# Optimization experiments

Measured on AMD Instinct MI355X. Metric: run time of the kernel, lower is better.

The kernel has to match this reference:

```python
import jax, jax.numpy as jnp
import numpy as np


def setup_inputs() -> dict:
    key = jax.random.key(0)
    ks = jax.random.split(key, 8)
    B, C, H, W = 4, 256, 64, 64
    Cqk = C // 8
    s = 0.05
    return {
        "x": jax.random.normal(ks[0], (B, C, H, W), jnp.float32),
        "Wq": jax.random.normal(ks[1], (Cqk, C), jnp.float32) * s,
        "bq": jax.random.normal(ks[2], (Cqk,), jnp.float32) * s,
        "Wk": jax.random.normal(ks[3], (Cqk, C), jnp.float32) * s,
        "bk": jax.random.normal(ks[4], (Cqk,), jnp.float32) * s,
        "Wv": jax.random.normal(ks[5], (C, C), jnp.float32) * s,
        "bv": jax.random.normal(ks[6], (C,), jnp.float32) * s,
        "gamma": jax.random.normal(ks[7], (1,), jnp.float32),
    }


def reference(x, Wq, bq, Wk, bk, Wv, bv, gamma):
    B, C, H, W = x.shape
    N = H * W
    xf = x.reshape(B, C, N)                      # [B,C,N]
    # 1x1 convs == channel matmuls
    q = jnp.einsum('oc,bcn->bon', Wq, xf) + bq[None, :, None]   # [B,C/8,N]
    k = jnp.einsum('oc,bcn->bon', Wk, xf) + bk[None, :, None]   # [B,C/8,N]
    v = jnp.einsum('oc,bcn->bon', Wv, xf) + bv[None, :, None]   # [B,C,N]
    # scores[b,i,j] = <q[:,i], k[:,j]>; softmax over j (last dim)
    scores = jnp.einsum('bci,bcj->bij', q, k)                   # [B,N,N]
    attn = jax.nn.softmax(scores, axis=-1)
    # out[b,c,i] = sum_j v[b,c,j] * attn[b,i,j]
    out = jnp.einsum('bcj,bij->bci', v, attn).reshape(B, C, H, W)
    return gamma[0] * out + x
```

## Files before the change

kernel.cpp:

```cpp
#include <hip/hip_runtime.h>


#define B_ 4
#define C_ 256
#define N_ 4096
#define CQK 32
#define LOG2E 1.44269504088896340736f

typedef __attribute__((ext_vector_type(8))) short short8;
typedef __attribute__((ext_vector_type(4))) short short4v;
typedef __attribute__((ext_vector_type(2))) unsigned int uint2v;
typedef __attribute__((ext_vector_type(16))) float f32x16;
typedef __attribute__((ext_vector_type(4))) float f32x4;

__device__ __forceinline__ unsigned short f2bf(float f) {
  unsigned int u = __builtin_bit_cast(unsigned int, f);
  u = (u + 0x7fffu + ((u >> 16) & 1u)) >> 16;
  return (unsigned short)u;
}
__device__ __forceinline__ float bf2f(unsigned short s) {
  unsigned int u = ((unsigned int)s) << 16;
  return __builtin_bit_cast(float, u);
}
__device__ __forceinline__ short f32tof16(float f) {
  const _Float16 hf = (_Float16)f;
  return __builtin_bit_cast(short, hf);
}
__device__ __forceinline__ unsigned int cvtpk(float lo, float hi) {
  unsigned int r;
  asm("v_cvt_pk_bf16_f32 %0, %1, %2" : "=v"(r) : "v"(lo), "v"(hi));
  return r;
}
__device__ __forceinline__ f32x16 mfma16(short8 a, short8 b, f32x16 c) {
  return __builtin_amdgcn_mfma_f32_32x32x16_bf16(a, b, c, 0, 0, 0);
}
__device__ __forceinline__ int swz64(int row, int col) {
  return row * 64 + ((((col >> 3) ^ row) & 7) << 3) + (col & 7);
}

#define WAITCNT(s) asm volatile("s_waitcnt " s ::: "memory")
#define BARRIER()                         \
  do {                                    \
    __builtin_amdgcn_s_barrier();         \
    asm volatile("" ::: "memory");        \
  } while (0)

__global__ __launch_bounds__(256) void k_prep(
    const float* __restrict__ x, unsigned short* __restrict__ xthi,
    unsigned short* __restrict__ xtlo,
    const float* __restrict__ Wq, const float* __restrict__ Wk,
    const float* __restrict__ Wv,
    unsigned short* __restrict__ wqh, unsigned short* __restrict__ wql,
    unsigned short* __restrict__ wkh, unsigned short* __restrict__ wkl,
    unsigned short* __restrict__ wvh, unsigned short* __restrict__ wvl) {
  __shared__ __align__(16) float tile[64 * 65];
  const int bi = blockIdx.x;
  const int t = threadIdx.x;
  if (bi < 1024) {
    const int it = bi & 63, ct = (bi >> 6) & 3, b = bi >> 8;
    const int i0 = it * 64, c0 = ct * 64;
    {
      const int i = t & 63, cb = t >> 6;
#pragma unroll
      for (int z = 0; z < 16; ++z) {
        const int c = z * 4 + cb;
        tile[i * 65 + c] = x[(b * C_ + c0 + c) * N_ + i0 + i];
      }
    }
    __syncthreads();
    {
      const int ii = t >> 2, p = t & 3;
      short8 h0, h1, l0, l1;
#pragma unroll
      for (int e = 0; e < 16; ++e) {
        const float f = tile[ii * 65 + p * 16 + e];
        const unsigned short hb = f2bf(f);
        const unsigned short lb = f2bf(f - bf2f(hb));
        if (e < 8) { h0[e] = (short)hb; l0[e] = (short)lb; }
        else       { h1[e - 8] = (short)hb; l1[e - 8] = (short)lb; }
      }
      const int base = (b * N_ + i0 + ii) * C_ + c0 + p * 16;
      *(short8*)(xthi + base) = h0;
      *(short8*)(xthi + base + 8) = h1;
      *(short8*)(xtlo + base) = l0;
      *(short8*)(xtlo + base + 8) = l1;
    }
  } else {
    const int e = (bi - 1024) * 256 + t;
    const float* src; unsigned short *hi, *lo; int idx;
    if (e < 8192)        { src = Wq; hi = wqh; lo = wql; idx = e; }
    else if (e < 16384)  { src = Wk; hi = wkh; lo = wkl; idx = e - 8192; }
    else                 { src = Wv; hi = wvh; lo = wvl; idx = e - 16384; }
    float f = src[idx];
    if (e < 8192) f *= LOG2E;
    const unsigned short h = f2bf(f);
    hi[idx] = h;
    lo[idx] = f2bf(f - bf2f(h));
  }
}

__global__ __launch_bounds__(256) void k_proj(
    const unsigned short* __restrict__ wqh, const unsigned short* __restrict__ wql,
    const unsigned short* __restrict__ wkh, const unsigned short* __restrict__ wkl,
    const unsigned short* __restrict__ wvh, const unsigned short* __restrict__ wvl,
    const unsigned short* __restrict__ xthi, const unsigned short* __restrict__ xtlo,
    const float* __restrict__ bq, const float* __restrict__ bk,
    const float* __restrict__ bv,
    unsigned short* __restrict__ qhg, unsigned short* __restrict__ qlg,
    unsigned short* __restrict__ khg, unsigned short* __restrict__ klg,
    unsigned short* __restrict__ vg) {
  __shared__ __align__(16) char sm[33792];
  unsigned short* awh = (unsigned short*)sm;
  unsigned short* awl = awh + 4096;
  unsigned short* bxh = awl + 4096;
  unsigned short* bxl = bxh + 4096;
  float* qt = (float*)sm;

  const int it = blockIdx.x, ot = blockIdx.y, b = blockIdx.z;
  const int i0 = it * 64, o0 = ot * 64;
  const int t = threadIdx.x, lane = t & 63, w = t >> 6, h = lane >> 5;
  const int mb = w >> 1, nb = w & 1;
  const int srow = t >> 2, sp = t & 3;

  const int og = o0 + srow;
  const unsigned short *wh, *wl;
  if (og < 32)      { wh = wqh + og * C_;        wl = wql + og * C_; }
  else if (og < 64) { wh = wkh + (og - 32) * C_; wl = wkl + (og - 32) * C_; }
  else              { wh = wvh + (og - 64) * C_; wl = wvl + (og - 64) * C_; }
  const unsigned short* xh = xthi + (b * N_ + i0 + srow) * C_;
  const unsigned short* xl = xtlo + (b * N_ + i0 + srow) * C_;

  f32x16 acc;
#pragma unroll
  for (int e = 0; e < 16; ++e) acc[e] = 0.f;
  const int m = 32 * mb + (lane & 31);
  const int n = 32 * nb + (lane & 31);

  for (int kt = 0; kt < 4; ++kt) {
    const int cb = kt * 64 + sp * 16;
    *(short8*)&awh[swz64(srow, sp * 16)]     = *(const short8*)(wh + cb);
    *(short8*)&awh[swz64(srow, sp * 16 + 8)] = *(const short8*)(wh + cb + 8);
    *(short8*)&awl[swz64(srow, sp * 16)]     = *(const short8*)(wl + cb);
    *(short8*)&awl[swz64(srow, sp * 16 + 8)] = *(const short8*)(wl + cb + 8);
    *(short8*)&bxh[swz64(srow, sp * 16)]     = *(const short8*)(xh + cb);
    *(short8*)&bxh[swz64(srow, sp * 16 + 8)] = *(const short8*)(xh + cb + 8);
    *(short8*)&bxl[swz64(srow, sp * 16)]     = *(const short8*)(xl + cb);
    *(short8*)&bxl[swz64(srow, sp * 16 + 8)] = *(const short8*)(xl + cb + 8);
    __syncthreads();
#pragma unroll
    for (int kk = 0; kk < 4; ++kk) {
      const int kb = kk * 16 + h * 8;
      const short8 ah  = *(const short8*)&awh[swz64(m, kb)];
      const short8 al2 = *(const short8*)&awl[swz64(m, kb)];
      const short8 bh  = *(const short8*)&bxh[swz64(n, kb)];
      const short8 bl2 = *(const short8*)&bxl[swz64(n, kb)];
      acc = mfma16(ah, bh, acc);
      acc = mfma16(ah, bl2, acc);
      acc = mfma16(al2, bh, acc);
    }
    __syncthreads();
  }

  if (ot > 0) {
#pragma unroll
    for (int e = 0; e < 16; ++e) {
      const int r = 32 * mb + (e & 3) + 8 * (e >> 2) + 4 * h;
      const int oc = o0 - 64 + r;
      vg[(b * C_ + oc) * N_ + i0 + n] = f2bf(acc[e] + bv[oc]);
    }
  } else {
#pragma unroll
    for (int e = 0; e < 16; ++e) {
      const int r = 32 * mb + (e & 3) + 8 * (e >> 2) + 4 * h;
      const float bias = (r < 32) ? bq[r] * LOG2E : bk[r - 32];
      qt[r * 65 + n] = acc[e] + bias;
    }
    __syncthreads();
    const int ii = t >> 2;
    short8 hv0, hv1, lv0, lv1;
#pragma unroll
    for (int e = 0; e < 16; ++e) {
      const float f = qt[(sp * 16 + e) * 65 + ii];
      const unsigned short hb = f2bf(f);
      const unsigned short lb = f2bf(f - bf2f(hb));
      if (e < 8) { hv0[e] = (short)hb; lv0[e] = (short)lb; }
      else       { hv1[e - 8] = (short)hb; lv1[e - 8] = (short)lb; }
    }
    if (sp < 2) {
      const int base = (b * N_ + i0 + ii) * CQK + sp * 16;
      *(short8*)(qhg + base) = hv0; *(short8*)(qhg + base + 8) = hv1;
      *(short8*)(qlg + base) = lv0; *(short8*)(qlg + base + 8) = lv1;
    } else {
      const int base = (b * N_ + i0 + ii) * CQK + sp * 16 - 32;
      *(short8*)(khg + base) = hv0; *(short8*)(khg + base + 8) = hv1;
      *(short8*)(klg + base) = lv0; *(short8*)(klg + base + 8) = lv1;
    }
  }
}

__global__ __launch_bounds__(384, 3) void k_flash(
    const unsigned short* __restrict__ qhg, const unsigned short* __restrict__ qlg,
    const unsigned short* __restrict__ khg, const unsigned short* __restrict__ klg,
    const unsigned short* __restrict__ vg,
    unsigned short* __restrict__ Opart, float* __restrict__ mlpart) {
  __shared__ __align__(16) char sm[16928];
  char* Pb0 = sm;
  char* Pb1 = sm + 8192;
  float* alphaA = (float*)(sm + 16384);
  float* chgF = (float*)(sm + 16896);

  const int blk = blockIdx.x;
  const int b = (blk >> 1) & 3;
  const int half = blk & 1;
  const int qt_ = blk >> 3;
  const int q0 = qt_ * 64;
  const int jbase = half * 2048;
  const int t = threadIdx.x, lane = t & 63, w = t >> 6, h = lane >> 5;
  const int l31 = lane & 31;

  if (w < 4) {
    const int c0 = 64 * w + l31;
    const unsigned short* vsrc0 = vg + (size_t)(b * C_ + c0) * N_ + jbase + h * 8;
    const unsigned short* vsrc1 = vsrc0 + (size_t)32 * N_;
    f32x16 acc0, acc1, acc2, acc3;
#pragma unroll
    for (int e = 0; e < 16; ++e) {
      acc0[e] = 0.f; acc1[e] = 0.f; acc2[e] = 0.f; acc3[e] = 0.f;
    }
    short8 vf0[4], vf1[4];
#pragma unroll
    for (int kk = 0; kk < 4; ++kk) {
      vf0[kk] = *(const short8*)(vsrc0 + kk * 16);
      vf1[kk] = *(const short8*)(vsrc1 + kk * 16);
    }
    WAITCNT("lgkmcnt(0)");
    BARRIER();

#pragma unroll 2
    for (int kt = 0; kt < 32; ++kt) {
      const char* pb = (kt & 1) ? Pb1 : Pb0;
      const float* alp = alphaA + (kt & 1) * 64;
      const float cA = chgF[(kt & 1) * 2];
      const float cB = chgF[(kt & 1) * 2 + 1];
      if (cA != 0.f) {
#pragma unroll
        for (int eq = 0; eq < 4; ++eq) {
          const f32x4 av = *(const f32x4*)(alp + 8 * eq + 4 * h);
#pragma unroll
          for (int q = 0; q < 4; ++q) {
            acc0[4 * eq + q] *= av[q];
            acc2[4 * eq + q] *= av[q];
          }
        }
      }
      if (cB != 0.f) {
#pragma unroll
        for (int eq = 0; eq < 4; ++eq) {
          const f32x4 av = *(const f32x4*)(alp + 32 + 8 * eq + 4 * h);
#pragma unroll
          for (int q = 0; q < 4; ++q) {
            acc1[4 * eq + q] *= av[q];
            acc3[4 * eq + q] *= av[q];
          }
        }
      }
      __builtin_amdgcn_s_setprio(1);
#pragma unroll
      for (int kk = 0; kk < 4; ++kk) {
        const int phys = (2 * kk + h) ^ (l31 & 7);
        const short8 pa0 = *(const short8*)(pb + l31 * 128 + phys * 16);
        const short8 pa1 = *(const short8*)(pb + (32 + l31) * 128 + phys * 16);
        acc0 = mfma16(pa0, vf0[kk], acc0);
        acc1 = mfma16(pa1, vf0[kk], acc1);
        acc2 = mfma16(pa0, vf1[kk], acc2);
        acc3 = mfma16(pa1, vf1[kk], acc3);
      }
      __builtin_amdgcn_s_setprio(0);
      if (kt + 1 < 32) {
#pragma unroll
        for (int kk = 0; kk < 4; ++kk) {
          vf0[kk] = *(const short8*)(vsrc0 + (kt + 1) * 64 + kk * 16);
          vf1[kk] = *(const short8*)(vsrc1 + (kt + 1) * 64 + kk * 16);
        }
      }
      WAITCNT("lgkmcnt(0)");
      BARRIER();
    }
    {
      unsigned short* dst = Opart + (size_t)blk * 16384 + (w * 64 + lane) * 64;
      short8 o[8];
#pragma unroll
      for (int e = 0; e < 8; ++e) {
        o[0][e] = f32tof16(acc0[e]);      o[1][e] = f32tof16(acc0[8 + e]);
        o[2][e] = f32tof16(acc1[e]);      o[3][e] = f32tof16(acc1[8 + e]);
        o[4][e] = f32tof16(acc2[e]);      o[5][e] = f32tof16(acc2[8 + e]);
        o[6][e] = f32tof16(acc3[e]);      o[7][e] = f32tof16(acc3[8 + e]);
      }
#pragma unroll
      for (int q = 0; q < 8; ++q) *(short8*)(dst + 8 * q) = o[q];
    }
  } else {
    const int sw = w - 4;
    const int srow = sw * 32 + l31;
    short8 qfh[2], qfl[2];
    {
      const unsigned short* qph = qhg + (size_t)(b * N_ + q0 + srow) * CQK + h * 8;
      const unsigned short* qpl = qlg + (size_t)(b * N_ + q0 + srow) * CQK + h * 8;
#pragma unroll
      for (int kk = 0; kk < 2; ++kk) {
        qfh[kk] = *(const short8*)(qph + kk * 16);
        qfl[kk] = *(const short8*)(qpl + kk * 16);
      }
    }
    const unsigned short* kph = khg + (size_t)(b * N_ + jbase + l31) * CQK + h * 8;
    const unsigned short* kpl = klg + (size_t)(b * N_ + jbase + l31) * CQK + h * 8;
    short8 kfh[2][2], kfl[2][2];
    float m_run = -1e30f, l_run = 0.f;

    auto loadK = [&](int tau) {
#pragma unroll
      for (int jt = 0; jt < 2; ++jt)
#pragma unroll
        for (int kk = 0; kk < 2; ++kk) {
          kfh[jt][kk] = *(const short8*)(kph + tau * 2048 + jt * 1024 + kk * 16);
          kfl[jt][kk] = *(const short8*)(kpl + tau * 2048 + jt * 1024 + kk * 16);
        }
    };
    auto s_step = [&](int tau) {
      f32x16 s0, s1;
#pragma unroll
      for (int e = 0; e < 16; ++e) { s0[e] = 0.f; s1[e] = 0.f; }
      __builtin_amdgcn_s_setprio(1);
#pragma unroll
      for (int kk = 0; kk < 2; ++kk) {
        s0 = mfma16(kfh[0][kk], qfh[kk], s0);
        s0 = mfma16(kfh[0][kk], qfl[kk], s0);
        s0 = mfma16(kfl[0][kk], qfh[kk], s0);
        s1 = mfma16(kfh[1][kk], qfh[kk], s1);
        s1 = mfma16(kfh[1][kk], qfl[kk], s1);
        s1 = mfma16(kfl[1][kk], qfh[kk], s1);
      }
      __builtin_amdgcn_s_setprio(0);
      if (tau + 1 < 32) loadK(tau + 1);
      float mx8[8];
#pragma unroll
      for (int i2 = 0; i2 < 4; ++i2) {
        mx8[i2] = fmaxf(fmaxf(s0[4 * i2], s0[4 * i2 + 1]),
                        fmaxf(s0[4 * i2 + 2], s0[4 * i2 + 3]));
        mx8[4 + i2] = fmaxf(fmaxf(s1[4 * i2], s1[4 * i2 + 1]),
                            fmaxf(s1[4 * i2 + 2], s1[4 * i2 + 3]));
      }
      float mx = fmaxf(fmaxf(fmaxf(mx8[0], mx8[1]), fmaxf(mx8[2], mx8[3])),
                       fmaxf(fmaxf(mx8[4], mx8[5]), fmaxf(mx8[6], mx8[7])));
      mx = fmaxf(mx, __shfl_xor(mx, 32));
      const float mnew = fmaxf(m_run, mx);
      const bool up = mnew > m_run;
      const float al = __builtin_exp2f(m_run - mnew);
#pragma unroll
      for (int e = 0; e < 16; ++e) s0[e] = __builtin_exp2f(s0[e] - mnew);
#pragma unroll
      for (int e = 0; e < 16; ++e) s1[e] = __builtin_exp2f(s1[e] - mnew);
      float t8[8];
#pragma unroll
      for (int i2 = 0; i2 < 4; ++i2) {
        t8[i2] = (s0[4 * i2] + s0[4 * i2 + 1]) + (s0[4 * i2 + 2] + s0[4 * i2 + 3]);
        t8[4 + i2] = (s1[4 * i2] + s1[4 * i2 + 1]) + (s1[4 * i2 + 2] + s1[4 * i2 + 3]);
      }
      float ts = ((t8[0] + t8[1]) + (t8[2] + t8[3])) +
                 ((t8[4] + t8[5]) + (t8[6] + t8[7]));
      ts += __shfl_xor(ts, 32);
      l_run = l_run * al + ts;
      char* Pw = (tau & 1) ? Pb1 : Pb0;
#pragma unroll
      for (int q = 0; q < 4; ++q) {
        uint2v u0, u1;
        u0[0] = cvtpk(s0[4 * q], s0[4 * q + 1]);
        u0[1] = cvtpk(s0[4 * q + 2], s0[4 * q + 3]);
        u1[0] = cvtpk(s1[4 * q], s1[4 * q + 1]);
        u1[1] = cvtpk(s1[4 * q + 2], s1[4 * q + 3]);
        const int ph0 = q ^ (srow & 7);
        const int ph1 = (4 + q) ^ (srow & 7);
        *(uint2v*)(Pw + srow * 128 + ph0 * 16 + 8 * h) = u0;
        *(uint2v*)(Pw + srow * 128 + ph1 * 16 + 8 * h) = u1;
      }
      const unsigned long long ba = __ballot(up);
      if (h == 0) alphaA[(tau & 1) * 64 + srow] = al;
      if (lane == 0) chgF[(tau & 1) * 2 + sw] = ba ? 1.f : 0.f;
      m_run = mnew;
    };

    loadK(0);
    s_step(0);
    WAITCNT("lgkmcnt(0)");
    BARRIER();
#pragma unroll 2
    for (int kt = 0; kt < 32; ++kt) {
      if (kt + 1 < 32) s_step(kt + 1);
      WAITCNT("lgkmcnt(0)");
      BARRIER();
    }
    if (h == 0) {
      mlpart[blk * 128 + srow] = m_run;
      mlpart[blk * 128 + 64 + srow] = l_run;
    }
  }
}

__global__ __launch_bounds__(256) void k_combine(
    const unsigned short* __restrict__ Opart, const float* __restrict__ mlpart,
    const float* __restrict__ x, const float* __restrict__ gamma,
    float* __restrict__ out) {
  const int cb = blockIdx.x;
  const int b = cb & 3, qt_ = cb >> 2;
  const int q0 = qt_ * 64;
  const int blk1 = (qt_ << 3) | (b << 1);
  const int blk2 = blk1 | 1;
  const int t = threadIdx.x;
  const int i = t & 63, cg = t >> 6;

  const float m1 = mlpart[blk1 * 128 + i], l1 = mlpart[blk1 * 128 + 64 + i];
  const float m2 = mlpart[blk2 * 128 + i], l2 = mlpart[blk2 * 128 + 64 + i];
  const float M = fmaxf(m1, m2);
  const float w1 = __builtin_exp2f(m1 - M), w2 = __builtin_exp2f(m2 - M);
  const float inv = 1.f / (w1 * l1 + w2 * l2);
  const float gm = gamma[0];
  const float s1 = gm * w1 * inv, s2 = gm * w2 * inv;

  const int hh = (i >> 2) & 1;
  const int e = (i & 3) + 4 * ((i >> 3) & 3);
  const int rs = i >> 5;
  const unsigned short* p1 = Opart + (size_t)blk1 * 16384;
  const unsigned short* p2 = Opart + (size_t)blk2 * 16384;
#pragma unroll 4
  for (int c = cg; c < C_; c += 4) {
    const int off = (c >> 6) * 4096 + ((c & 31) + 32 * hh) * 64 +
                    (rs + 2 * ((c >> 5) & 1)) * 16 + e;
    const float o1 = (float)__builtin_bit_cast(_Float16, p1[off]);
    const float o2 = (float)__builtin_bit_cast(_Float16, p2[off]);
    const int g = (b * C_ + c) * N_ + q0 + i;
    out[g] = s1 * o1 + s2 * o2 + x[g];
  }
}

extern "C" void kernel_launch(void* const* d_in, const int* in_sizes, int n_in,
                              void* d_out, int out_size, void* d_ws, size_t ws_size,
                              hipStream_t stream) {
  const float* x     = (const float*)d_in[0];
  const float* Wq    = (const float*)d_in[1];
  const float* bq    = (const float*)d_in[2];
  const float* Wk    = (const float*)d_in[3];
  const float* bk    = (const float*)d_in[4];
  const float* Wv    = (const float*)d_in[5];
  const float* bv    = (const float*)d_in[6];
  const float* gamma = (const float*)d_in[7];
  float* out = (float*)d_out;
  (void)in_sizes; (void)n_in; (void)out_size; (void)ws_size;

  char* ws = (char*)d_ws;
  size_t off = 0;
  auto carve = [&](size_t bytes) -> char* {
    char* p = ws + off;
    off += (bytes + 255) & ~(size_t)255;
    return p;
  };
  unsigned short* xthi = (unsigned short*)carve((size_t)B_ * N_ * C_ * 2);
  unsigned short* xtlo = (unsigned short*)carve((size_t)B_ * N_ * C_ * 2);
  unsigned short* wqh  = (unsigned short*)carve(32 * 256 * 2);
  unsigned short* wql  = (unsigned short*)carve(32 * 256 * 2);
  unsigned short* wkh  = (unsigned short*)carve(32 * 256 * 2);
  unsigned short* wkl  = (unsigned short*)carve(32 * 256 * 2);
  unsigned short* wvh  = (unsigned short*)carve(256 * 256 * 2);
  unsigned short* wvl  = (unsigned short*)carve(256 * 256 * 2);
  unsigned short* qhg  = (unsigned short*)carve((size_t)B_ * N_ * CQK * 2);
  unsigned short* qlg  = (unsigned short*)carve((size_t)B_ * N_ * CQK * 2);
  unsigned short* khg  = (unsigned short*)carve((size_t)B_ * N_ * CQK * 2);
  unsigned short* klg  = (unsigned short*)carve((size_t)B_ * N_ * CQK * 2);
  unsigned short* vg   = (unsigned short*)carve((size_t)B_ * C_ * N_ * 2);
  unsigned short* Opart = (unsigned short*)carve((size_t)512 * 16384 * 2);
  float* mlpart = (float*)carve((size_t)512 * 128 * 4);

  k_prep<<<1344, 256, 0, stream>>>(x, xthi, xtlo, Wq, Wk, Wv,
                                   wqh, wql, wkh, wkl, wvh, wvl);
  k_proj<<<dim3(64, 5, B_), 256, 0, stream>>>(wqh, wql, wkh, wkl, wvh, wvl,
                                              xthi, xtlo, bq, bk, bv,
                                              qhg, qlg, khg, klg, vg);
  k_flash<<<512, 384, 0, stream>>>(qhg, qlg, khg, klg, vg, Opart, mlpart);
  k_combine<<<256, 256, 0, stream>>>(Opart, mlpart, x, gamma, out);
}
```

Measured before the change: 187.9 us.

## Fuse score and PV stages per wave, passing P through registers instead of LDS

Replaces the producer/consumer warp specialization (2 score waves writing P to LDS, 4 PV waves reading it with block barriers) with self-contained waves. Each wave computes its own 32-row score tile, converts P to bf16 in registers via lane shuffles, and feeds it directly into the PV MFMAs for 128 channels. This removes the LDS P buffers and the per-step barriers. In exchange, scores are recomputed twice per query row (once per channel half) and V loads are no longer prefetched. The Opart/mlpart layouts and the combine kernel's indexing are reworked to match.

```diff
diff --git a/kernel.cpp b/kernel.cpp
--- a/kernel.cpp
+++ b/kernel.cpp
@@ -9,7 +9,7 @@
 
 typedef __attribute__((ext_vector_type(8))) short short8;
 typedef __attribute__((ext_vector_type(4))) short short4v;
-typedef __attribute__((ext_vector_type(2))) unsigned int uint2v;
+typedef __attribute__((ext_vector_type(4))) unsigned int uint4v;
 typedef __attribute__((ext_vector_type(16))) float f32x16;
 typedef __attribute__((ext_vector_type(4))) float f32x4;
 
@@ -37,13 +37,6 @@
 __device__ __forceinline__ int swz64(int row, int col) {
   return row * 64 + ((((col >> 3) ^ row) & 7) << 3) + (col & 7);
 }
-
-#define WAITCNT(s) asm volatile("s_waitcnt " s ::: "memory")
-#define BARRIER()                         \
-  do {                                    \
-    __builtin_amdgcn_s_barrier();         \
-    asm volatile("" ::: "memory");        \
-  } while (0)
 
 __global__ __launch_bounds__(256) void k_prep(
     const float* __restrict__ x, unsigned short* __restrict__ xthi,
@@ -198,211 +191,219 @@
   }
 }
 
-__global__ __launch_bounds__(384, 3) void k_flash(
+__global__ __launch_bounds__(256, 2) void k_flash(
     const unsigned short* __restrict__ qhg, const unsigned short* __restrict__ qlg,
     const unsigned short* __restrict__ khg, const unsigned short* __restrict__ klg,
     const unsigned short* __restrict__ vg,
     unsigned short* __restrict__ Opart, float* __restrict__ mlpart) {
-  __shared__ __align__(16) char sm[16928];
-  char* Pb0 = sm;
-  char* Pb1 = sm + 8192;
-  float* alphaA = (float*)(sm + 16384);
-  float* chgF = (float*)(sm + 16896);
+  __shared__ float alphaW[4][32];
 
   const int blk = blockIdx.x;
-  const int b = (blk >> 1) & 3;
-  const int half = blk & 1;
-  const int qt_ = blk >> 3;
-  const int q0 = qt_ * 64;
-  const int jbase = half * 2048;
+  const int xs = blk & 7;
+  const int b = xs >> 1, s = xs & 1;
+  const int gl = blk >> 3;
   const int t = threadIdx.x, lane = t & 63, w = t >> 6, h = lane >> 5;
   const int l31 = lane & 31;
-
-  if (w < 4) {
-    const int c0 = 64 * w + l31;
-    const unsigned short* vsrc0 = vg + (size_t)(b * C_ + c0) * N_ + jbase + h * 8;
-    const unsigned short* vsrc1 = vsrc0 + (size_t)32 * N_;
-    f32x16 acc0, acc1, acc2, acc3;
-#pragma unroll
-    for (int e = 0; e < 16; ++e) {
-      acc0[e] = 0.f; acc1[e] = 0.f; acc2[e] = 0.f; acc3[e] = 0.f;
-    }
-    short8 vf0[4], vf1[4];
-#pragma unroll
-    for (int kk = 0; kk < 4; ++kk) {
-      vf0[kk] = *(const short8*)(vsrc0 + kk * 16);
-      vf1[kk] = *(const short8*)(vsrc1 + kk * 16);
-    }
-    WAITCNT("lgkmcnt(0)");
-    BARRIER();
-
-#pragma unroll 2
-    for (int kt = 0; kt < 32; ++kt) {
-      const char* pb = (kt & 1) ? Pb1 : Pb0;
-      const float* alp = alphaA + (kt & 1) * 64;
-      const float cA = chgF[(kt & 1) * 2];
-      const float cB = chgF[(kt & 1) * 2 + 1];
-      if (cA != 0.f) {
-#pragma unroll
-        for (int eq = 0; eq < 4; ++eq) {
-          const f32x4 av = *(const f32x4*)(alp + 8 * eq + 4 * h);
-#pragma unroll
-          for (int q = 0; q < 4; ++q) {
-            acc0[4 * eq + q] *= av[q];
-            acc2[4 * eq + q] *= av[q];
-          }
+  const int widx = gl * 4 + w;
+  const int qw = widx >> 1, ch = widx & 1;
+  const int srow = qw * 32 + l31;
+  const int jbase = s * 2048;
+
+  short8 qfh[2], qfl[2];
+  {
+    const unsigned short* qph = qhg + (size_t)(b * N_ + srow) * CQK + h * 8;
+    const unsigned short* qpl = qlg + (size_t)(b * N_ + srow) * CQK + h * 8;
+#pragma unroll
+    for (int kk = 0; kk < 2; ++kk) {
+      qfh[kk] = *(const short8*)(qph + kk * 16);
+      qfl[kk] = *(const short8*)(qpl + kk * 16);
+    }
+  }
+  const unsigned short* kph = khg + (size_t)(b * N_ + jbase + l31) * CQK + h * 8;
+  const unsigned short* kpl = klg + (size_t)(b * N_ + jbase + l31) * CQK + h * 8;
+  short8 kfh[2][2], kfl[2][2];
+  auto loadK = [&](int tau) {
+#pragma unroll
+    for (int jt = 0; jt < 2; ++jt)
+#pragma unroll
+      for (int kk = 0; kk < 2; ++kk) {
+        kfh[jt][kk] = *(const short8*)(kph + tau * 2048 + jt * 1024 + kk * 16);
+        kfl[jt][kk] = *(const short8*)(kpl + tau * 2048 + jt * 1024 + kk * 16);
+      }
+  };
+  loadK(0);
+  const unsigned short* vsr0 =
+      vg + (size_t)(b * C_ + ch * 128 + l31) * N_ + jbase + h * 8;
+
+  f32x16 acc0, acc1, acc2, acc3;
+#pragma unroll
+  for (int e = 0; e < 16; ++e) {
+    acc0[e] = 0.f; acc1[e] = 0.f; acc2[e] = 0.f; acc3[e] = 0.f;
+  }
+  float m_run = -1e30f, l_run = 0.f;
+
+  for (int kt = 0; kt < 32; ++kt) {
+    short8 vf0[4], vf1[4], vf2[4], vf3[4];
+#pragma unroll
+    for (int sl = 0; sl < 4; ++sl) {
+      vf0[sl] = *(const short8*)(vsr0 + (size_t)0 * 32 * N_ + kt * 64 + sl * 16);
+      vf1[sl] = *(const short8*)(vsr0 + (size_t)1 * 32 * N_ + kt * 64 + sl * 16);
+      vf2[sl] = *(const short8*)(vsr0 + (size_t)2 * 32 * N_ + kt * 64 + sl * 16);
+      vf3[sl] = *(const short8*)(vsr0 + (size_t)3 * 32 * N_ + kt * 64 + sl * 16);
+    }
+    f32x16 s0, s1;
+#pragma unroll
+    for (int e = 0; e < 16; ++e) { s0[e] = 0.f; s1[e] = 0.f; }
+    __builtin_amdgcn_s_setprio(1);
+#pragma unroll
+    for (int kk = 0; kk < 2; ++kk) {
+      s0 = mfma16(kfh[0][kk], qfh[kk], s0);
+      s0 = mfma16(kfh[0][kk], qfl[kk], s0);
+      s0 = mfma16(kfl[0][kk], qfh[kk], s0);
+      s1 = mfma16(kfh[1][kk], qfh[kk], s1);
+      s1 = mfma16(kfh[1][kk], qfl[kk], s1);
+      s1 = mfma16(kfl[1][kk], qfh[kk], s1);
+    }
+    __builtin_amdgcn_s_setprio(0);
+    if (kt + 1 < 32) loadK(kt + 1);
+    float mx8[8];
+#pragma unroll
+    for (int i2 = 0; i2 < 4; ++i2) {
+      mx8[i2] = fmaxf(fmaxf(s0[4 * i2], s0[4 * i2 + 1]),
+                      fmaxf(s0[4 * i2 + 2], s0[4 * i2 + 3]));
+      mx8[4 + i2] = fmaxf(fmaxf(s1[4 * i2], s1[4 * i2 + 1]),
+                          fmaxf(s1[4 * i2 + 2], s1[4 * i2 + 3]));
+    }
+    float mx = fmaxf(fmaxf(fmaxf(mx8[0], mx8[1]), fmaxf(mx8[2], mx8[3])),
+                     fmaxf(fmaxf(mx8[4], mx8[5]), fmaxf(mx8[6], mx8[7])));
+    mx = fmaxf(mx, __shfl_xor(mx, 32));
+    const float mnew = fmaxf(m_run, mx);
+    const unsigned long long ba = __ballot(mnew > m_run);
+    const float al = __builtin_exp2f(m_run - mnew);
+#pragma unroll
+    for (int e = 0; e < 16; ++e) s0[e] = __builtin_exp2f(s0[e] - mnew);
+#pragma unroll
+    for (int e = 0; e < 16; ++e) s1[e] = __builtin_exp2f(s1[e] - mnew);
+    float t8[8];
+#pragma unroll
+    for (int i2 = 0; i2 < 4; ++i2) {
+      t8[i2] = (s0[4 * i2] + s0[4 * i2 + 1]) + (s0[4 * i2 + 2] + s0[4 * i2 + 3]);
+      t8[4 + i2] = (s1[4 * i2] + s1[4 * i2 + 1]) + (s1[4 * i2 + 2] + s1[4 * i2 + 3]);
+    }
+    float ts = ((t8[0] + t8[1]) + (t8[2] + t8[3])) +
+               ((t8[4] + t8[5]) + (t8[6] + t8[7]));
+    ts += __shfl_xor(ts, 32);
+    l_run = l_run * al + ts;
+    m_run = mnew;
+    short8 pa0, pa1, pa2, pa3;
+    {
+      unsigned int w01 = cvtpk(s0[0], s0[1]),  w23 = cvtpk(s0[2], s0[3]);
+      unsigned int w45 = cvtpk(s0[4], s0[5]),  w67 = cvtpk(s0[6], s0[7]);
+      unsigned int w89 = cvtpk(s0[8], s0[9]),  wab = cvtpk(s0[10], s0[11]);
+      unsigned int wcd = cvtpk(s0[12], s0[13]), wef = cvtpk(s0[14], s0[15]);
+      unsigned int t01 = (unsigned)__shfl_xor((int)w01, 32);
+      unsigned int t23 = (unsigned)__shfl_xor((int)w23, 32);
+      unsigned int t45 = (unsigned)__shfl_xor((int)w45, 32);
+      unsigned int t67 = (unsigned)__shfl_xor((int)w67, 32);
+      unsigned int t89 = (unsigned)__shfl_xor((int)w89, 32);
+      unsigned int tab = (unsigned)__shfl_xor((int)wab, 32);
+      unsigned int tcd = (unsigned)__shfl_xor((int)wcd, 32);
+      unsigned int tef = (unsigned)__shfl_xor((int)wef, 32);
+      uint4v uA, uB;
+      uA[0] = h ? t45 : w01;  uA[1] = h ? t67 : w23;
+      uA[2] = h ? w45 : t01;  uA[3] = h ? w67 : t23;
+      uB[0] = h ? tcd : w89;  uB[1] = h ? tef : wab;
+      uB[2] = h ? wcd : t89;  uB[3] = h ? wef : tab;
+      pa0 = __builtin_bit_cast(short8, uA);
+      pa1 = __builtin_bit_cast(short8, uB);
+    }
+    {
+      unsigned int w01 = cvtpk(s1[0], s1[1]),  w23 = cvtpk(s1[2], s1[3]);
+      unsigned int w45 = cvtpk(s1[4], s1[5]),  w67 = cvtpk(s1[6], s1[7]);
+      unsigned int w89 = cvtpk(s1[8], s1[9]),  wab = cvtpk(s1[10], s1[11]);
+      unsigned int wcd = cvtpk(s1[12], s1[13]), wef = cvtpk(s1[14], s1[15]);
+      unsigned int t01 = (unsigned)__shfl_xor((int)w01, 32);
+      unsigned int t23 = (unsigned)__shfl_xor((int)w23, 32);
+      unsigned int t45 = (unsigned)__shfl_xor((int)w45, 32);
+      unsigned int t67 = (unsigned)__shfl_xor((int)w67, 32);
+      unsigned int t89 = (unsigned)__shfl_xor((int)w89, 32);
+      unsigned int tab = (unsigned)__shfl_xor((int)wab, 32);
+      unsigned int tcd = (unsigned)__shfl_xor((int)wcd, 32);
+      unsigned int tef = (unsigned)__shfl_xor((int)wef, 32);
+      uint4v uA, uB;
+      uA[0] = h ? t45 : w01;  uA[1] = h ? t67 : w23;
+      uA[2] = h ? w45 : t01;  uA[3] = h ? w67 : t23;
+      uB[0] = h ? tcd : w89;  uB[1] = h ? tef : wab;
+      uB[2] = h ? wcd : t89;  uB[3] = h ? wef : tab;
+      pa2 = __builtin_bit_cast(short8, uA);
+      pa3 = __builtin_bit_cast(short8, uB);
+    }
+    if (ba) {
+      if (h == 0) alphaW[w][l31] = al;
+#pragma unroll
+      for (int eq = 0; eq < 4; ++eq) {
+        const f32x4 av = *(const f32x4*)&alphaW[w][8 * eq + 4 * h];
+#pragma unroll
+        for (int q = 0; q < 4; ++q) {
+          acc0[4 * eq + q] *= av[q];
+          acc1[4 * eq + q] *= av[q];
+          acc2[4 * eq + q] *= av[q];
+          acc3[4 * eq + q] *= av[q];
         }
       }
-      if (cB != 0.f) {
-#pragma unroll
-        for (int eq = 0; eq < 4; ++eq) {
-          const f32x4 av = *(const f32x4*)(alp + 32 + 8 * eq + 4 * h);
-#pragma unroll
-          for (int q = 0; q < 4; ++q) {
-            acc1[4 * eq + q] *= av[q];
-            acc3[4 * eq + q] *= av[q];
-          }
-        }
-      }
-      __builtin_amdgcn_s_setprio(1);
-#pragma unroll
-      for (int kk = 0; kk < 4; ++kk) {
-        const int phys = (2 * kk + h) ^ (l31 & 7);
-        const short8 pa0 = *(const short8*)(pb + l31 * 128 + phys * 16);
-        const short8 pa1 = *(const short8*)(pb + (32 + l31) * 128 + phys * 16);
-        acc0 = mfma16(pa0, vf0[kk], acc0);
-        acc1 = mfma16(pa1, vf0[kk], acc1);
-        acc2 = mfma16(pa0, vf1[kk], acc2);
-        acc3 = mfma16(pa1, vf1[kk], acc3);
-      }
-      __builtin_amdgcn_s_setprio(0);
-      if (kt + 1 < 32) {
-#pragma unroll
-        for (int kk = 0; kk < 4; ++kk) {
-          vf0[kk] = *(const short8*)(vsrc0 + (kt + 1) * 64 + kk * 16);
-          vf1[kk] = *(const short8*)(vsrc1 + (kt + 1) * 64 + kk * 16);
-        }
-      }
-      WAITCNT("lgkmcnt(0)");
-      BARRIER();
-    }
-    {
-      unsigned short* dst = Opart + (size_t)blk * 16384 + (w * 64 + lane) * 64;
-      short8 o[8];
-#pragma unroll
-      for (int e = 0; e < 8; ++e) {
-        o[0][e] = f32tof16(acc0[e]);      o[1][e] = f32tof16(acc0[8 + e]);
-        o[2][e] = f32tof16(acc1[e]);      o[3][e] = f32tof16(acc1[8 + e]);
-        o[4][e] = f32tof16(acc2[e]);      o[5][e] = f32tof16(acc2[8 + e]);
-        o[6][e] = f32tof16(acc3[e]);      o[7][e] = f32tof16(acc3[8 + e]);
-      }
-#pragma unroll
-      for (int q = 0; q < 8; ++q) *(short8*)(dst + 8 * q) = o[q];
-    }
-  } else {
-    const int sw = w - 4;
-    const int srow = sw * 32 + l31;
-    short8 qfh[2], qfl[2];
-    {
-      const unsigned short* qph = qhg + (size_t)(b * N_ + q0 + srow) * CQK + h * 8;
-      const unsigned short* qpl = qlg + (size_t)(b * N_ + q0 + srow) * CQK + h * 8;
-#pragma unroll
-      for (int kk = 0; kk < 2; ++kk) {
-        qfh[kk] = *(const short8*)(qph + kk * 16);
-        qfl[kk] = *(const short8*)(qpl + kk * 16);
-      }
-    }
-    const unsigned short* kph = khg + (size_t)(b * N_ + jbase + l31) * CQK + h * 8;
-    const unsigned short* kpl = klg + (size_t)(b * N_ + jbase + l31) * CQK + h * 8;
-    short8 kfh[2][2], kfl[2][2];
-    float m_run = -1e30f, l_run = 0.f;
-
-    auto loadK = [&](int tau) {
-#pragma unroll
-      for (int jt = 0; jt < 2; ++jt)
-#pragma unroll
-        for (int kk = 0; kk < 2; ++kk) {
-          kfh[jt][kk] = *(const short8*)(kph + tau * 2048 + jt * 1024 + kk * 16);
-          kfl[jt][kk] = *(const short8*)(kpl + tau * 2048 + jt * 1024 + kk * 16);
-        }
-    };
-    auto s_step = [&](int tau) {
-      f32x16 s0, s1;
-#pragma unroll
-      for (int e = 0; e < 16; ++e) { s0[e] = 0.f; s1[e] = 0.f; }
-      __builtin_amdgcn_s_setprio(1);
-#pragma unroll
-      for (int kk = 0; kk < 2; ++kk) {
-        s0 = mfma16(kfh[0][kk], qfh[kk], s0);
-        s0 = mfma16(kfh[0][kk], qfl[kk], s0);
-        s0 = mfma16(kfl[0][kk], qfh[kk], s0);
-        s1 = mfma16(kfh[1][kk], qfh[kk], s1);
-        s1 = mfma16(kfh[1][kk], qfl[kk], s1);
-        s1 = mfma16(kfl[1][kk], qfh[kk], s1);
-      }
-      __builtin_amdgcn_s_setprio(0);
-      if (tau + 1 < 32) loadK(tau + 1);
-      float mx8[8];
-#pragma unroll
-      for (int i2 = 0; i2 < 4; ++i2) {
-        mx8[i2] = fmaxf(fmaxf(s0[4 * i2], s0[4 * i2 + 1]),
-                        fmaxf(s0[4 * i2 + 2], s0[4 * i2 + 3]));
-        mx8[4 + i2] = fmaxf(fmaxf(s1[4 * i2], s1[4 * i2 + 1]),
-                            fmaxf(s1[4 * i2 + 2], s1[4 * i2 + 3]));
-      }
-      float mx = fmaxf(fmaxf(fmaxf(mx8[0], mx8[1]), fmaxf(mx8[2], mx8[3])),
-                       fmaxf(fmaxf(mx8[4], mx8[5]), fmaxf(mx8[6], mx8[7])));
-      mx = fmaxf(mx, __shfl_xor(mx, 32));
-      const float mnew = fmaxf(m_run, mx);
-      const bool up = mnew > m_run;
-      const float al = __builtin_exp2f(m_run - mnew);
-#pragma unroll
-      for (int e = 0; e < 16; ++e) s0[e] = __builtin_exp2f(s0[e] - mnew);
-#pragma unroll
-      for (int e = 0; e < 16; ++e) s1[e] = __builtin_exp2f(s1[e] - mnew);
-      float t8[8];
-#pragma unroll
-      for (int i2 = 0; i2 < 4; ++i2) {
-        t8[i2] = (s0[4 * i2] + s0[4 * i2 + 1]) + (s0[4 * i2 + 2] + s0[4 * i2 + 3]);
-        t8[4 + i2] = (s1[4 * i2] + s1[4 * i2 + 1]) + (s1[4 * i2 + 2] + s1[4 * i2 + 3]);
-      }
-      float ts = ((t8[0] + t8[1]) + (t8[2] + t8[3])) +
-                 ((t8[4] + t8[5]) + (t8[6] + t8[7]));
-      ts += __shfl_xor(ts, 32);
-      l_run = l_run * al + ts;
-      char* Pw = (tau & 1) ? Pb1 : Pb0;
-#pragma unroll
-      for (int q = 0; q < 4; ++q) {
-        uint2v u0, u1;
-        u0[0] = cvtpk(s0[4 * q], s0[4 * q + 1]);
-        u0[1] = cvtpk(s0[4 * q + 2], s0[4 * q + 3]);
-        u1[0] = cvtpk(s1[4 * q], s1[4 * q + 1]);
-        u1[1] = cvtpk(s1[4 * q + 2], s1[4 * q + 3]);
-        const int ph0 = q ^ (srow & 7);
-        const int ph1 = (4 + q) ^ (srow & 7);
-        *(uint2v*)(Pw + srow * 128 + ph0 * 16 + 8 * h) = u0;
-        *(uint2v*)(Pw + srow * 128 + ph1 * 16 + 8 * h) = u1;
-      }
-      const unsigned long long ba = __ballot(up);
-      if (h == 0) alphaA[(tau & 1) * 64 + srow] = al;
-      if (lane == 0) chgF[(tau & 1) * 2 + sw] = ba ? 1.f : 0.f;
-      m_run = mnew;
-    };
-
-    loadK(0);
-    s_step(0);
-    WAITCNT("lgkmcnt(0)");
-    BARRIER();
-#pragma unroll 2
-    for (int kt = 0; kt < 32; ++kt) {
-      if (kt + 1 < 32) s_step(kt + 1);
-      WAITCNT("lgkmcnt(0)");
-      BARRIER();
-    }
-    if (h == 0) {
-      mlpart[blk * 128 + srow] = m_run;
-      mlpart[blk * 128 + 64 + srow] = l_run;
-    }
+    }
+    __builtin_amdgcn_s_setprio(1);
+    acc0 = mfma16(pa0, vf0[0], acc0);
+    acc0 = mfma16(pa1, vf0[1], acc0);
+    acc0 = mfma16(pa2, vf0[2], acc0);
+    acc0 = mfma16(pa3, vf0[3], acc0);
+    acc1 = mfma16(pa0, vf1[0], acc1);
+    acc1 = mfma16(pa1, vf1[1], acc1);
+    acc1 = mfma16(pa2, vf1[2], acc1);
+    acc1 = mfma16(pa3, vf1[3], acc1);
+    acc2 = mfma16(pa0, vf2[0], acc2);
+    acc2 = mfma16(pa1, vf2[1], acc2);
+    acc2 = mfma16(pa2, vf2[2], acc2);
+    acc2 = mfma16(pa3, vf2[3], acc2);
+    acc3 = mfma16(pa0, vf3[0], acc3);
+    acc3 = mfma16(pa1, vf3[1], acc3);
+    acc3 = mfma16(pa2, vf3[2], acc3);
+    acc3 = mfma16(pa3, vf3[3], acc3);
+    __builtin_amdgcn_s_setprio(0);
+  }
+
+  if (ch == 0 && h == 0) {
+    mlpart[((size_t)(s * 4 + b) * 4096 + srow) * 2] = m_run;
+    mlpart[((size_t)(s * 4 + b) * 4096 + srow) * 2 + 1] = l_run;
+  }
+  {
+    const int wv = ((s * 4 + b) * 128 + qw) * 2 + ch;
+    unsigned short* dst = Opart + (size_t)wv * 4096 + lane * 8;
+    short8 o;
+#pragma unroll
+    for (int e = 0; e < 8; ++e) o[e] = f32tof16(acc0[e]);
+    *(short8*)(dst + 0 * 512) = o;
+#pragma unroll
+    for (int e = 0; e < 8; ++e) o[e] = f32tof16(acc0[8 + e]);
+    *(short8*)(dst + 1 * 512) = o;
+#pragma unroll
+    for (int e = 0; e < 8; ++e) o[e] = f32tof16(acc1[e]);
+    *(short8*)(dst + 2 * 512) = o;
+#pragma unroll
+    for (int e = 0; e < 8; ++e) o[e] = f32tof16(acc1[8 + e]);
+    *(short8*)(dst + 3 * 512) = o;
+#pragma unroll
+    for (int e = 0; e < 8; ++e) o[e] = f32tof16(acc2[e]);
+    *(short8*)(dst + 4 * 512) = o;
+#pragma unroll
+    for (int e = 0; e < 8; ++e) o[e] = f32tof16(acc2[8 + e]);
+    *(short8*)(dst + 5 * 512) = o;
+#pragma unroll
+    for (int e = 0; e < 8; ++e) o[e] = f32tof16(acc3[e]);
+    *(short8*)(dst + 6 * 512) = o;
+#pragma unroll
+    for (int e = 0; e < 8; ++e) o[e] = f32tof16(acc3[8 + e]);
+    *(short8*)(dst + 7 * 512) = o;
   }
 }
 
@@ -413,32 +414,35 @@
   const int cb = blockIdx.x;
   const int b = cb & 3, qt_ = cb >> 2;
   const int q0 = qt_ * 64;
-  const int blk1 = (qt_ << 3) | (b << 1);
-  const int blk2 = blk1 | 1;
   const int t = threadIdx.x;
   const int i = t & 63, cg = t >> 6;
-
-  const float m1 = mlpart[blk1 * 128 + i], l1 = mlpart[blk1 * 128 + 64 + i];
-  const float m2 = mlpart[blk2 * 128 + i], l2 = mlpart[blk2 * 128 + 64 + i];
+  const int qg = q0 + i;
+
+  const float m1 = mlpart[((size_t)(0 + b) * 4096 + qg) * 2];
+  const float l1 = mlpart[((size_t)(0 + b) * 4096 + qg) * 2 + 1];
+  const float m2 = mlpart[((size_t)(4 + b) * 4096 + qg) * 2];
+  const float l2 = mlpart[((size_t)(4 + b) * 4096 + qg) * 2 + 1];
   const float M = fmaxf(m1, m2);
   const float w1 = __builtin_exp2f(m1 - M), w2 = __builtin_exp2f(m2 - M);
-  const float inv = 1.f / (w1 * l1 + w2 * l2);
-  const float gm = gamma[0];
-  const float s1 = gm * w1 * inv, s2 = gm * w2 * inv;
-
-  const int hh = (i >> 2) & 1;
-  const int e = (i & 3) + 4 * ((i >> 3) & 3);
-  const int rs = i >> 5;
-  const unsigned short* p1 = Opart + (size_t)blk1 * 16384;
-  const unsigned short* p2 = Opart + (size_t)blk2 * 16384;
+  const float inv = gamma[0] / (w1 * l1 + w2 * l2);
+  const float s1 = w1 * inv, s2 = w2 * inv;
+
+  const int qw = qg >> 5, qi = qg & 31;
+  const int h = (qi >> 2) & 1;
+  const int hi8 = qi >> 4;
+  const int eo = (qi & 3) + 4 * ((qi >> 3) & 1);
 #pragma unroll 4
   for (int c = cg; c < C_; c += 4) {
-    const int off = (c >> 6) * 4096 + ((c & 31) + 32 * hh) * 64 +
-                    (rs + 2 * ((c >> 5) & 1)) * 16 + e;
-    const float o1 = (float)__builtin_bit_cast(_Float16, p1[off]);
-    const float o2 = (float)__builtin_bit_cast(_Float16, p2[off]);
-    const int g = (b * C_ + c) * N_ + q0 + i;
-    out[g] = s1 * o1 + s2 * o2 + x[g];
+    const int ch = c >> 7, ct = (c >> 5) & 3, ln = (c & 31) + 32 * h;
+    const size_t sub = (size_t)(ct * 2 + hi8) * 512 + ln * 8 + eo;
+    const size_t o1 =
+        (size_t)(((0 + b) * 128 + qw) * 2 + ch) * 4096 + sub;
+    const size_t o2 =
+        (size_t)(((4 + b) * 128 + qw) * 2 + ch) * 4096 + sub;
+    const float v1 = (float)__builtin_bit_cast(_Float16, Opart[o1]);
+    const float v2 = (float)__builtin_bit_cast(_Float16, Opart[o2]);
+    const int g = (b * C_ + c) * N_ + qg;
+    out[g] = s1 * v1 + s2 * v2 + x[g];
   }
 }
 
@@ -476,14 +480,14 @@
   unsigned short* khg  = (unsigned short*)carve((size_t)B_ * N_ * CQK * 2);
   unsigned short* klg  = (unsigned short*)carve((size_t)B_ * N_ * CQK * 2);
   unsigned short* vg   = (unsigned short*)carve((size_t)B_ * C_ * N_ * 2);
-  unsigned short* Opart = (unsigned short*)carve((size_t)512 * 16384 * 2);
-  float* mlpart = (float*)carve((size_t)512 * 128 * 4);
+  unsigned short* Opart = (unsigned short*)carve((size_t)2048 * 4096 * 2);
+  float* mlpart = (float*)carve((size_t)8 * 4096 * 2 * 4);
 
   k_prep<<<1344, 256, 0, stream>>>(x, xthi, xtlo, Wq, Wk, Wv,
                                    wqh, wql, wkh, wkl, wvh, wvl);
   k_proj<<<dim3(64, 5, B_), 256, 0, stream>>>(wqh, wql, wkh, wkl, wvh, wvl,
                                               xthi, xtlo, bq, bk, bv,
                                               qhg, qlg, khg, klg, vg);
-  k_flash<<<512, 384, 0, stream>>>(qhg, qlg, khg, klg, vg, Opart, mlpart);
+  k_flash<<<512, 256, 0, stream>>>(qhg, qlg, khg, klg, vg, Opart, mlpart);
   k_combine<<<256, 256, 0, stream>>>(Opart, mlpart, x, gamma, out);
 }
```

Result: slower. 283.2 us (+50.7%).
